# Performance work log

Hardware: AMD Instinct MI355X
Metric: run time of the kernel (lower is better)

The kernel has to match this reference:

```python
import jax, jax.numpy as jnp
import numpy as np

ALPHA = 1.5      # entmax parameter from __init__
N_ITER = 50      # bisection iterations (converges well past fp32 precision)


def entmax_bisect(x, alpha=ALPHA, n_iter=N_ITER):
    """alpha-entmax along the last axis via bisection on the threshold tau.
    p_i = ((alpha-1)*x_i - tau)_+ ** (1/(alpha-1)), with sum_i p_i = 1.
    """
    q = 1.0 / (alpha - 1.0)
    z = x * (alpha - 1.0)
    mx = jnp.max(z, axis=-1, keepdims=True)
    # tau is bracketed by [mx - 1, mx]: sum >= 1 at lo, sum = 0 at hi
    lo, hi = mx - 1.0, mx

    def body(_, carry):
        lo, hi = carry
        tau = 0.5 * (lo + hi)
        f = jnp.sum(jnp.maximum(z - tau, 0.0) ** q, axis=-1, keepdims=True) - 1.0
        lo = jnp.where(f > 0.0, tau, lo)
        hi = jnp.where(f > 0.0, hi, tau)
        return lo, hi

    lo, hi = jax.lax.fori_loop(0, n_iter, body, (lo, hi))
    tau = 0.5 * (lo + hi)
    p = jnp.maximum(z - tau, 0.0) ** q
    return p / jnp.sum(p, axis=-1, keepdims=True)  # exact renormalization


def setup_inputs() -> dict:
    key = jax.random.key(0)
    kq, kk, kv = jax.random.split(key, 3)
    B, T, D = 16, 2048, 256
    return {
        "query": jax.random.normal(kq, (B, T, D), dtype=jnp.float32),
        "value": jax.random.normal(kv, (B, T, D), dtype=jnp.float32),
        "key": jax.random.normal(kk, (B, T, D), dtype=jnp.float32),
    }


def reference(query, value, key):
    # scores: [B, Tq, Tk]
    scores = jnp.einsum("btd,bsd->bts", query, key)
    weights = entmax_bisect(scores)          # sparse attention weights
    return jnp.einsum("bts,bsd->btd", weights, value)
```

## Files before the change

kernel.cpp:

```cpp
#include <hip/hip_runtime.h>

#define TT 2048
#define DD 256
#define RQB 128
#define NT 512
#define KB 128
#define NTILE (TT / KB)
#define NITER 30
#define CAP 28

#define L_CIDX 131072
#define L_CVAL (L_CIDX + RQB * CAP * 2)
#define L_CNT  (L_CVAL + RQB * CAP * 4)
#define L_SLOT (L_CNT + RQB * 4)
#define L_OVF  (L_SLOT + 8 * 16 * CAP * 2)
#define LDS_SZ (L_OVF + 16)

typedef __attribute__((ext_vector_type(4))) float f32x4;
typedef __attribute__((ext_vector_type(8))) short short8;

__device__ inline unsigned short f2bf(float x) {
    unsigned u = __float_as_uint(x);
    return (unsigned short)((u + 0x7fffu + ((u >> 16) & 1u)) >> 16);
}
__device__ inline float bf2f(unsigned short h) {
    return __uint_as_float((unsigned)h << 16);
}

__device__ __forceinline__ void gload16(const void* g, void* l) {
    __builtin_amdgcn_global_load_lds(
        (const __attribute__((address_space(1))) void*)g,
        (__attribute__((address_space(3))) void*)l, 16, 0, 0);
}

__device__ __forceinline__ float dppmax16(float m) {
    int a = __builtin_amdgcn_update_dpp(__float_as_int(m), __float_as_int(m),
                                        0xB1, 0xF, 0xF, false);
    m = fmaxf(m, __int_as_float(a));
    a = __builtin_amdgcn_update_dpp(__float_as_int(m), __float_as_int(m),
                                    0x4E, 0xF, 0xF, false);
    m = fmaxf(m, __int_as_float(a));
    a = __builtin_amdgcn_update_dpp(__float_as_int(m), __float_as_int(m),
                                    0x141, 0xF, 0xF, false);
    m = fmaxf(m, __int_as_float(a));
    a = __builtin_amdgcn_update_dpp(__float_as_int(m), __float_as_int(m),
                                    0x140, 0xF, 0xF, false);
    m = fmaxf(m, __int_as_float(a));
    return m;
}

__global__ __launch_bounds__(256) void split_k_kernel(const float* __restrict__ K,
        unsigned short* __restrict__ Kh, int n4) {
    int i = blockIdx.x * 256 + threadIdx.x;
    const int stride = gridDim.x * 256;
    for (; i < n4; i += stride) {
        float4 v = ((const float4*)K)[i];
        unsigned short h0 = f2bf(0.5f * v.x), h1 = f2bf(0.5f * v.y);
        unsigned short h2 = f2bf(0.5f * v.z), h3 = f2bf(0.5f * v.w);
        uint2 hv;
        hv.x = (unsigned)h0 | ((unsigned)h1 << 16);
        hv.y = (unsigned)h2 | ((unsigned)h3 << 16);
        ((uint2*)Kh)[i] = hv;
    }
}

__launch_bounds__(NT, 2)
__global__ void entmax_screen_kernel(const float* __restrict__ Q,
                                     const unsigned short* __restrict__ Kh,
                                     const float* __restrict__ Kf,
                                     const float* __restrict__ V,
                                     float* __restrict__ Out,
                                     int nwg) {
    extern __shared__ char smem[];
    unsigned short* CIDX = (unsigned short*)(smem + L_CIDX);
    float*          CVAL = (float*)(smem + L_CVAL);
    int*            CNT  = (int*)(smem + L_CNT);
    unsigned short* SLOT = (unsigned short*)(smem + L_SLOT);
    int*            POVF = (int*)(smem + L_OVF);

    const int tid = threadIdx.x;
    const int wid = tid >> 6, lane = tid & 63;
    const int l15 = lane & 15, ag = lane >> 4;
    const int wrow0 = wid * 16;

    const int lb = (blockIdx.x & 7) * (nwg >> 3) + (blockIdx.x >> 3);
    const int b  = lb >> 4;
    const int t0 = (lb & 15) * RQB;

    const char* KhB = (const char*)(Kh + (size_t)b * TT * DD);

    if (tid == 0) *POVF = 0;

    short8 ah[8];
    {
        const float* qr = Q + (size_t)(b * TT + t0 + wrow0 + l15) * DD;
        #pragma unroll
        for (int kk = 0; kk < 8; ++kk) {
            const int d0 = kk * 32 + ag * 8;
            float4 qa = *(const float4*)(qr + d0);
            float4 qb = *(const float4*)(qr + d0 + 4);
            float qf[8] = {qa.x, qa.y, qa.z, qa.w, qb.x, qb.y, qb.z, qb.w};
            #pragma unroll
            for (int i = 0; i < 8; ++i) ah[kk][i] = (short)f2bf(qf[i]);
        }
    }

    auto STAGE = [&](int tile, int buf) {
        #pragma unroll
        for (int j = 0; j < 8; ++j) {
            const int ofs = wid * 8192 + j * 1024 + lane * 16;
            const int cl = ofs >> 9, wb = ofs & 511;
            const size_t gb = ((size_t)((tile << 7) + cl) << 9) +
                              (size_t)(wb ^ ((cl & 7) << 4));
            gload16(KhB + gb, smem + buf * 65536 + wid * 8192 + j * 1024);
        }
    };

    STAGE(0, 0);
    __syncthreads();

    const unsigned long long grpmask = 0xFFFFULL << (ag * 16);
    const unsigned long long lowmask = (lane == 0) ? 0ULL : ((~0ULL) >> (64 - lane));
    float rmax[4];
    int   base[4];
    #pragma unroll
    for (int r = 0; r < 4; ++r) { rmax[r] = -3.402823466e38f; base[r] = 0; }

    for (int t = 0; t < NTILE; ++t) {
        const int cur = t & 1;
        if (t + 1 < NTILE) STAGE(t + 1, cur ^ 1);
        f32x4 acc[8];
        #pragma unroll
        for (int ct = 0; ct < 8; ++ct)
            #pragma unroll
            for (int r = 0; r < 4; ++r) acc[ct][r] = 0.0f;
        #pragma unroll
        for (int kk = 0; kk < 8; ++kk) {
            short8 bh[8];
            #pragma unroll
            for (int ct = 0; ct < 8; ++ct)
                bh[ct] = *(const short8*)(smem + cur * 65536 + (ct * 16 + l15) * 512 +
                                          (((kk * 64) + ag * 16) ^ ((l15 & 7) << 4)));
            #pragma unroll
            for (int ct = 0; ct < 8; ++ct)
                acc[ct] = __builtin_amdgcn_mfma_f32_16x16x32_bf16(ah[kk], bh[ct], acc[ct], 0, 0, 0);
        }
        #pragma unroll
        for (int rg = 0; rg < 4; ++rg) {
            float m = acc[0][rg];
            #pragma unroll
            for (int ct = 1; ct < 8; ++ct) m = fmaxf(m, acc[ct][rg]);
            m = dppmax16(m);
            rmax[rg] = fmaxf(rmax[rg], m);
            const float thr = rmax[rg] - 1.6f;
            if (m > thr) {
                const int row = wrow0 + ag * 4 + rg;
                #pragma unroll
                for (int ct = 0; ct < 8; ++ct) {
                    const bool p = acc[ct][rg] > thr;
                    const unsigned long long ball = __ballot(p) & grpmask;
                    if (ball) {
                        const int rank = (int)__popcll(ball & lowmask);
                        if (p && base[rg] + rank < CAP)
                            CIDX[row * CAP + base[rg] + rank] =
                                (unsigned short)((t << 7) + ct * 16 + l15);
                        base[rg] += (int)__popcll(ball);
                    }
                }
            }
        }
        __syncthreads();
    }

    #pragma unroll
    for (int rg = 0; rg < 4; ++rg) {
        if (l15 == 0) {
            CNT[wrow0 + ag * 4 + rg] = base[rg];
            if (base[rg] > CAP) *POVF = 1;
        }
    }
    __syncthreads();

    int c = 0;
    if (lane < 16) {
        const int cc = CNT[wrow0 + lane];
        c = cc > CAP ? CAP : cc;
    }
    int x = c;
    #pragma unroll
    for (int off = 1; off < 16; off <<= 1) {
        const int v = __shfl_up(x, off);
        if ((lane & 15) >= off) x += v;
    }
    const int pfx = x - c;
    const int total = __shfl(x, 15);
    if (lane < 16)
        for (int i = 0; i < c; ++i)
            SLOT[wid * (16 * CAP) + pfx + i] = (unsigned short)((lane << 8) | i);
    __syncthreads();

    {
        const float* Qb = Q + (size_t)(b * TT + t0 + wrow0) * DD;
        const float* Kb = Kf + (size_t)b * TT * DD;
        for (int bs = 0; bs < total; bs += 8) {
            float4 qv[8], kv[8];
            int rl[8], ii[8];
            #pragma unroll
            for (int u = 0; u < 8; ++u) {
                const int s = bs + u;
                const int e = (s < total) ? (int)SLOT[wid * (16 * CAP) + s] : 0;
                rl[u] = e >> 8; ii[u] = e & 255;
                const int col = (s < total) ? (int)CIDX[(wrow0 + rl[u]) * CAP + ii[u]] : 0;
                qv[u] = *(const float4*)(Qb + (size_t)rl[u] * DD + lane * 4);
                kv[u] = *(const float4*)(Kb + (size_t)col * DD + lane * 4);
            }
            float sm[8];
            #pragma unroll
            for (int u = 0; u < 8; ++u) {
                float d = qv[u].x * kv[u].x;
                d = fmaf(qv[u].y, kv[u].y, d);
                d = fmaf(qv[u].z, kv[u].z, d);
                d = fmaf(qv[u].w, kv[u].w, d);
                sm[u] = d;
            }
            #pragma unroll
            for (int off = 32; off; off >>= 1)
                #pragma unroll
                for (int u = 0; u < 8; ++u) sm[u] += __shfl_xor(sm[u], off);
            #pragma unroll
            for (int u = 0; u < 8; ++u)
                if (lane == u && bs + u < total)
                    CVAL[(wrow0 + rl[u]) * CAP + ii[u]] = 0.5f * sm[u];
        }
    }
    __syncthreads();

    if (*POVF) {
        if (wid == 0) {
            float* fbz = (float*)smem;
            for (int r = 0; r < RQB; ++r) {
                if (CNT[r] <= CAP) continue;
                const float* qr = Q + (size_t)(b * TT + t0 + r) * DD;
                const float* Kb = Kf + (size_t)b * TT * DD;
                for (int cc2 = lane; cc2 < TT; cc2 += 64) {
                    const float* kr = Kb + (size_t)cc2 * DD;
                    float a = 0.0f;
                    for (int d = 0; d < DD; ++d) a = fmaf(qr[d], kr[d], a);
                    fbz[cc2] = 0.5f * a;
                }
                __threadfence_block();
                float m = -3.402823466e38f;
                for (int cc2 = lane; cc2 < TT; cc2 += 64) m = fmaxf(m, fbz[cc2]);
                #pragma unroll
                for (int off = 32; off; off >>= 1) m = fmaxf(m, __shfl_xor(m, off));
                float lo = m - 1.0f, hi = m, tau;
                for (int it = 0; it < NITER; ++it) {
                    tau = 0.5f * (lo + hi);
                    float s = 0.0f;
                    for (int cc2 = lane; cc2 < TT; cc2 += 64) {
                        const float tt2 = fmaxf(fbz[cc2] - tau, 0.0f);
                        s = fmaf(tt2, tt2, s);
                    }
                    #pragma unroll
                    for (int off = 32; off; off >>= 1) s += __shfl_xor(s, off);
                    const bool gt = s > 1.0f;
                    lo = gt ? tau : lo;
                    hi = gt ? hi : tau;
                }
                tau = 0.5f * (lo + hi);
                float ssum = 0.0f;
                for (int cc2 = lane; cc2 < TT; cc2 += 64) {
                    const float tt2 = fmaxf(fbz[cc2] - tau, 0.0f);
                    ssum = fmaf(tt2, tt2, ssum);
                }
                #pragma unroll
                for (int off = 32; off; off >>= 1) ssum += __shfl_xor(ssum, off);
                const float inv = 1.0f / ssum;
                const int d4 = lane * 4;
                float4 o = make_float4(0.f, 0.f, 0.f, 0.f);
                for (int s = 0; s < TT; ++s) {
                    const float tt2 = fmaxf(fbz[s] - tau, 0.0f);
                    const float w = tt2 * tt2 * inv;
                    if (w > 0.0f) {
                        const float4 v = *(const float4*)(V + ((size_t)b * TT + s) * DD + d4);
                        o.x = fmaf(w, v.x, o.x); o.y = fmaf(w, v.y, o.y);
                        o.z = fmaf(w, v.z, o.z); o.w = fmaf(w, v.w, o.w);
                    }
                }
                *(float4*)(Out + ((size_t)(b * TT + t0 + r)) * DD + d4) = o;
                if (lane == 0) CNT[r] = -1;
                __threadfence_block();
            }
        }
        __syncthreads();
    }

    {
        const int myrow = wrow0 + (lane & 15);
        const int nRaw = CNT[myrow];
        const int n = (nRaw < 0) ? 0 : (nRaw > CAP ? CAP : nRaw);
        float cvr[CAP];
        #pragma unroll
        for (int i = 0; i < CAP; ++i)
            cvr[i] = (i < n) ? CVAL[myrow * CAP + i] : -3.0e30f;
        float emax = cvr[0];
        #pragma unroll
        for (int i = 1; i < CAP; ++i) emax = fmaxf(emax, cvr[i]);
        float lo = emax - 1.0f, hi = emax;
        for (int it = 0; it < NITER; ++it) {
            const float tau = 0.5f * (lo + hi);
            float s = 0.0f;
            #pragma unroll
            for (int i = 0; i < CAP; ++i) {
                const float tt2 = fmaxf(cvr[i] - tau, 0.0f);
                s = fmaf(tt2, tt2, s);
            }
            const bool gt = s > 1.0f;
            lo = gt ? tau : lo;
            hi = gt ? hi : tau;
        }
        const float tau = 0.5f * (lo + hi);
        float ssum = 0.0f;
        #pragma unroll
        for (int i = 0; i < CAP; ++i) {
            const float tt2 = fmaxf(cvr[i] - tau, 0.0f);
            ssum = fmaf(tt2, tt2, ssum);
        }
        const float inv = 1.0f / ssum;
        if (lane < 16 && n > 0) {
            for (int i = 0; i < n; ++i) {
                const float tt2 = fmaxf(cvr[i] - tau, 0.0f);
                CVAL[myrow * CAP + i] = tt2 * tt2 * inv;
            }
        }
    }

    const float* Vb = V + (size_t)b * TT * DD;
    for (int j = 0; j < 16; ++j) {
        const int row = wrow0 + j;
        const int n = CNT[row];
        if (n < 0) continue;
        const int d4 = lane * 4;
        float4 o = make_float4(0.f, 0.f, 0.f, 0.f);
        for (int i = 0; i < n; ++i) {
            const float wi = CVAL[row * CAP + i];
            if (wi > 0.0f) {
                const int si = (int)CIDX[row * CAP + i];
                const float4 v = *(const float4*)(Vb + (size_t)si * DD + d4);
                o.x = fmaf(wi, v.x, o.x); o.y = fmaf(wi, v.y, o.y);
                o.z = fmaf(wi, v.z, o.z); o.w = fmaf(wi, v.w, o.w);
            }
        }
        *(float4*)(Out + ((size_t)(b * TT + t0 + row)) * DD + d4) = o;
    }
}

#define DOT4(A, Kv, Qv) \
    A = fmaf((Qv).x, (Kv).x, fmaf((Qv).y, (Kv).y, fmaf((Qv).z, (Kv).z, fmaf((Qv).w, (Kv).w, (A)))))

__launch_bounds__(256, 2)
__global__ void entmax_fallback_kernel(const float* __restrict__ Q,
                                       const float* __restrict__ V,
                                       const float* __restrict__ K,
                                       float* __restrict__ Out) {
    extern __shared__ float zshf[];
    const int tid = threadIdx.x;
    const int b   = blockIdx.x >> 8;
    const int t0  = (blockIdx.x & 255) * 8;
    const float* Qb = Q + ((size_t)b * TT + t0) * DD;
    const float* Kb = K + (size_t)b * TT * DD;
    const float* Vb = V + (size_t)b * TT * DD;
    for (int g = 0; g < 2; ++g) {
        const int c0 = (g << 10) + tid;
        const float* k0 = Kb + (size_t)c0 * DD;
        float4 acc[8];
        #pragma unroll
        for (int r = 0; r < 8; ++r) acc[r] = make_float4(0.f, 0.f, 0.f, 0.f);
        for (int d = 0; d < DD; d += 4) {
            const float4 ka = *(const float4*)(k0 + d);
            const float4 kb = *(const float4*)(k0 + 256 * DD + d);
            const float4 kc = *(const float4*)(k0 + 512 * DD + d);
            const float4 kd = *(const float4*)(k0 + 768 * DD + d);
            #pragma unroll
            for (int r = 0; r < 8; ++r) {
                const float4 qv = *(const float4*)(Qb + r * DD + d);
                DOT4(acc[r].x, ka, qv); DOT4(acc[r].y, kb, qv);
                DOT4(acc[r].z, kc, qv); DOT4(acc[r].w, kd, qv);
            }
        }
        #pragma unroll
        for (int r = 0; r < 8; ++r) {
            zshf[r * TT + c0      ] = 0.5f * acc[r].x;
            zshf[r * TT + c0 + 256] = 0.5f * acc[r].y;
            zshf[r * TT + c0 + 512] = 0.5f * acc[r].z;
            zshf[r * TT + c0 + 768] = 0.5f * acc[r].w;
        }
    }
    __syncthreads();
    {
        const int wid = tid >> 6, lane = tid & 63;
        for (int rr = 0; rr < 2; ++rr) {
            const int r = wid * 2 + rr;
            float* z = zshf + r * TT;
            float zv[32];
            float m = -3.402823466e38f;
            #pragma unroll
            for (int j = 0; j < 32; ++j) { zv[j] = z[lane + (j << 6)]; m = fmaxf(m, zv[j]); }
            #pragma unroll
            for (int off = 32; off; off >>= 1) m = fmaxf(m, __shfl_xor(m, off));
            float lo = m - 1.0f, hi = m;
            for (int it = 0; it < NITER; ++it) {
                const float tau = 0.5f * (lo + hi);
                float s = 0.f;
                #pragma unroll
                for (int j = 0; j < 32; ++j) { float t = fmaxf(zv[j] - tau, 0.f); s = fmaf(t, t, s); }
                #pragma unroll
                for (int off = 32; off; off >>= 1) s += __shfl_xor(s, off);
                const bool gt = (s - 1.0f) > 0.0f;
                lo = gt ? tau : lo; hi = gt ? hi : tau;
            }
            const float tau = 0.5f * (lo + hi);
            float ssum = 0.f;
            #pragma unroll
            for (int j = 0; j < 32; ++j) { float t = fmaxf(zv[j] - tau, 0.f); ssum = fmaf(t, t, ssum); }
            #pragma unroll
            for (int off = 32; off; off >>= 1) ssum += __shfl_xor(ssum, off);
            const float inv = 1.0f / ssum;
            #pragma unroll
            for (int j = 0; j < 32; ++j) {
                float t = fmaxf(zv[j] - tau, 0.f);
                z[lane + (j << 6)] = t * t * inv;
            }
        }
    }
    __syncthreads();
    {
        const int d2 = (tid & 127) * 2;
        const int sg = tid >> 7;
        float2 acc[8];
        #pragma unroll
        for (int r = 0; r < 8; ++r) acc[r] = make_float2(0.f, 0.f);
        for (int sc = 0; sc < TT; sc += 8) {
            const int s0 = sc + sg * 4;
            float4 w4[8];
            #pragma unroll
            for (int r = 0; r < 8; ++r) w4[r] = *(const float4*)&zshf[r * TT + s0];
            #pragma unroll
            for (int js = 0; js < 4; ++js) {
                const float2 v = *(const float2*)(Vb + (size_t)(s0 + js) * DD + d2);
                #pragma unroll
                for (int r = 0; r < 8; ++r) {
                    const float wv = (js == 0) ? w4[r].x : (js == 1) ? w4[r].y
                                   : (js == 2) ? w4[r].z : w4[r].w;
                    acc[r].x = fmaf(wv, v.x, acc[r].x);
                    acc[r].y = fmaf(wv, v.y, acc[r].y);
                }
            }
        }
        __syncthreads();
        float* part = zshf;
        if (sg == 1) {
            #pragma unroll
            for (int r = 0; r < 8; ++r) *(float2*)&part[r * DD + d2] = acc[r];
        }
        __syncthreads();
        if (sg == 0) {
            #pragma unroll
            for (int r = 0; r < 8; ++r) {
                const float2 p = *(const float2*)&part[r * DD + d2];
                float2 o; o.x = acc[r].x + p.x; o.y = acc[r].y + p.y;
                *(float2*)&Out[((size_t)b * TT + t0 + r) * DD + d2] = o;
            }
        }
    }
}

extern "C" void kernel_launch(void* const* d_in, const int* in_sizes, int n_in,
                              void* d_out, int out_size, void* d_ws, size_t ws_size,
                              hipStream_t stream) {
    const float* Q = (const float*)d_in[0];
    const float* V = (const float*)d_in[1];
    const float* K = (const float*)d_in[2];
    float* Out = (float*)d_out;
    const int B = in_sizes[0] / (TT * DD);
    const size_t NE = (size_t)B * TT * DD;
    const size_t need = NE * 2;

    if (ws_size < need) {
        entmax_fallback_kernel<<<dim3(B * (TT / 8)), 256, 8 * TT * sizeof(float), stream>>>(
            Q, V, K, Out);
        return;
    }

    unsigned short* Kh = (unsigned short*)d_ws;
    split_k_kernel<<<2048, 256, 0, stream>>>(K, Kh, (int)(NE / 4));

    const int nwg = B * (TT / RQB);
    (void)hipFuncSetAttribute((const void*)entmax_screen_kernel,
                              hipFuncAttributeMaxDynamicSharedMemorySize, LDS_SZ);
    entmax_screen_kernel<<<dim3(nwg), NT, LDS_SZ, stream>>>(Q, Kh, K, V, Out, nwg);
}
```

Baseline: 135.0 us.

## Triple-buffer smaller K tiles with prefetch depth two and fine-grained waits

```diff
diff --git a/kernel.cpp b/kernel.cpp
--- a/kernel.cpp
+++ b/kernel.cpp
@@ -4,12 +4,12 @@
 #define DD 256
 #define RQB 128
 #define NT 512
-#define KB 128
+#define KB 64
 #define NTILE (TT / KB)
 #define NITER 30
 #define CAP 28
 
-#define L_CIDX 131072
+#define L_CIDX 98304
 #define L_CVAL (L_CIDX + RQB * CAP * 2)
 #define L_CNT  (L_CVAL + RQB * CAP * 4)
 #define L_SLOT (L_CNT + RQB * 4)
@@ -22,9 +22,6 @@
 __device__ inline unsigned short f2bf(float x) {
     unsigned u = __float_as_uint(x);
     return (unsigned short)((u + 0x7fffu + ((u >> 16) & 1u)) >> 16);
-}
-__device__ inline float bf2f(unsigned short h) {
-    return __uint_as_float((unsigned)h << 16);
 }
 
 __device__ __forceinline__ void gload16(const void* g, void* l) {
@@ -105,19 +102,25 @@
         }
     }
 
+    int gofs[4], lofs[4];
+    #pragma unroll
+    for (int j = 0; j < 4; ++j) {
+        const int ofs = wid * 4096 + j * 1024 + lane * 16;
+        const int cl = ofs >> 9, wb = ofs & 511;
+        gofs[j] = cl * 512 + (wb ^ ((cl & 7) << 4));
+        lofs[j] = ofs;
+    }
     auto STAGE = [&](int tile, int buf) {
-        #pragma unroll
-        for (int j = 0; j < 8; ++j) {
-            const int ofs = wid * 8192 + j * 1024 + lane * 16;
-            const int cl = ofs >> 9, wb = ofs & 511;
-            const size_t gb = ((size_t)((tile << 7) + cl) << 9) +
-                              (size_t)(wb ^ ((cl & 7) << 4));
-            gload16(KhB + gb, smem + buf * 65536 + wid * 8192 + j * 1024);
-        }
+        const size_t gt = (size_t)tile << 15;
+        char* lb_ = smem + buf * 32768;
+        #pragma unroll
+        for (int j = 0; j < 4; ++j) gload16(KhB + gt + gofs[j], lb_ + lofs[j]);
     };
 
     STAGE(0, 0);
-    __syncthreads();
+    STAGE(1, 1);
+    asm volatile("s_waitcnt vmcnt(4)" ::: "memory");
+    __builtin_amdgcn_s_barrier();
 
     const unsigned long long grpmask = 0xFFFFULL << (ag * 16);
     const unsigned long long lowmask = (lane == 0) ? 0ULL : ((~0ULL) >> (64 - lane));
@@ -126,50 +129,60 @@
     #pragma unroll
     for (int r = 0; r < 4; ++r) { rmax[r] = -3.402823466e38f; base[r] = 0; }
 
+    int bufc = 0;
     for (int t = 0; t < NTILE; ++t) {
-        const int cur = t & 1;
-        if (t + 1 < NTILE) STAGE(t + 1, cur ^ 1);
-        f32x4 acc[8];
-        #pragma unroll
-        for (int ct = 0; ct < 8; ++ct)
+        if (t + 2 < NTILE) {
+            int sb = bufc + 2; if (sb >= 3) sb -= 3;
+            STAGE(t + 2, sb);
+        }
+        f32x4 acc[4];
+        #pragma unroll
+        for (int ct = 0; ct < 4; ++ct)
             #pragma unroll
             for (int r = 0; r < 4; ++r) acc[ct][r] = 0.0f;
+        __builtin_amdgcn_s_setprio(1);
         #pragma unroll
         for (int kk = 0; kk < 8; ++kk) {
-            short8 bh[8];
-            #pragma unroll
-            for (int ct = 0; ct < 8; ++ct)
-                bh[ct] = *(const short8*)(smem + cur * 65536 + (ct * 16 + l15) * 512 +
+            short8 bh[4];
+            #pragma unroll
+            for (int ct = 0; ct < 4; ++ct)
+                bh[ct] = *(const short8*)(smem + bufc * 32768 + (ct * 16 + l15) * 512 +
                                           (((kk * 64) + ag * 16) ^ ((l15 & 7) << 4)));
             #pragma unroll
-            for (int ct = 0; ct < 8; ++ct)
+            for (int ct = 0; ct < 4; ++ct)
                 acc[ct] = __builtin_amdgcn_mfma_f32_16x16x32_bf16(ah[kk], bh[ct], acc[ct], 0, 0, 0);
         }
+        __builtin_amdgcn_s_setprio(0);
         #pragma unroll
         for (int rg = 0; rg < 4; ++rg) {
-            float m = acc[0][rg];
-            #pragma unroll
-            for (int ct = 1; ct < 8; ++ct) m = fmaxf(m, acc[ct][rg]);
+            float m = fmaxf(fmaxf(acc[0][rg], acc[1][rg]), fmaxf(acc[2][rg], acc[3][rg]));
             m = dppmax16(m);
             rmax[rg] = fmaxf(rmax[rg], m);
             const float thr = rmax[rg] - 1.6f;
             if (m > thr) {
                 const int row = wrow0 + ag * 4 + rg;
                 #pragma unroll
-                for (int ct = 0; ct < 8; ++ct) {
+                for (int ct = 0; ct < 4; ++ct) {
                     const bool p = acc[ct][rg] > thr;
                     const unsigned long long ball = __ballot(p) & grpmask;
                     if (ball) {
                         const int rank = (int)__popcll(ball & lowmask);
                         if (p && base[rg] + rank < CAP)
                             CIDX[row * CAP + base[rg] + rank] =
-                                (unsigned short)((t << 7) + ct * 16 + l15);
+                                (unsigned short)((t << 6) + ct * 16 + l15);
                         base[rg] += (int)__popcll(ball);
                     }
                 }
             }
         }
-        __syncthreads();
+        if (t + 2 < NTILE) {
+            asm volatile("s_waitcnt vmcnt(4)" ::: "memory");
+            __builtin_amdgcn_s_barrier();
+        } else if (t + 2 == NTILE) {
+            asm volatile("s_waitcnt vmcnt(0)" ::: "memory");
+            __builtin_amdgcn_s_barrier();
+        }
+        if (++bufc == 3) bufc = 0;
     }
 
     #pragma unroll
```

After: 145.9 us. +8.1%, slower.

## Switch screening GEMM to 32x32x16 MFMA with 2x2 wave tiling and per-wave candidate merge

Applied to the files above, without the earlier changes.

```diff
diff --git a/kernel.cpp b/kernel.cpp
--- a/kernel.cpp
+++ b/kernel.cpp
@@ -7,24 +7,26 @@
 #define KB 128
 #define NTILE (TT / KB)
 #define NITER 30
-#define CAP 28
-
-#define L_CIDX 131072
-#define L_CVAL (L_CIDX + RQB * CAP * 2)
-#define L_CNT  (L_CVAL + RQB * CAP * 4)
-#define L_SLOT (L_CNT + RQB * 4)
-#define L_OVF  (L_SLOT + 8 * 16 * CAP * 2)
+#define CAPW 20
+#define CAP 40
+#define SLACK 1.6f
+
+#define L_IW   131072
+#define L_CIDX (L_IW + 8 * 32 * CAPW * 2)
+#define L_CW   (L_CIDX + RQB * CAP * 2)
+#define L_OVF  (L_CW + 1024)
 #define LDS_SZ (L_OVF + 16)
-
-typedef __attribute__((ext_vector_type(4))) float f32x4;
+#define L_CVAL 0
+#define L_SLOT 20480
+#define L_CNT  30720
+#define L_FBZ  36864
+
+typedef __attribute__((ext_vector_type(16))) float f32x16;
 typedef __attribute__((ext_vector_type(8))) short short8;
 
 __device__ inline unsigned short f2bf(float x) {
     unsigned u = __float_as_uint(x);
     return (unsigned short)((u + 0x7fffu + ((u >> 16) & 1u)) >> 16);
-}
-__device__ inline float bf2f(unsigned short h) {
-    return __uint_as_float((unsigned)h << 16);
 }
 
 __device__ __forceinline__ void gload16(const void* g, void* l) {
@@ -65,126 +67,156 @@
 }
 
 __launch_bounds__(NT, 2)
-__global__ void entmax_screen_kernel(const float* __restrict__ Q,
-                                     const unsigned short* __restrict__ Kh,
-                                     const float* __restrict__ Kf,
-                                     const float* __restrict__ V,
-                                     float* __restrict__ Out,
-                                     int nwg) {
+__global__ void entmax32_kernel(const float* __restrict__ Q,
+                                const unsigned short* __restrict__ Kh,
+                                const float* __restrict__ Kf,
+                                const float* __restrict__ V,
+                                float* __restrict__ Out,
+                                int nwg) {
     extern __shared__ char smem[];
+    unsigned short* IW   = (unsigned short*)(smem + L_IW);
     unsigned short* CIDX = (unsigned short*)(smem + L_CIDX);
+    int*            CW   = (int*)(smem + L_CW);
+    int*            POVF = (int*)(smem + L_OVF);
     float*          CVAL = (float*)(smem + L_CVAL);
+    unsigned short* SLOT = (unsigned short*)(smem + L_SLOT);
     int*            CNT  = (int*)(smem + L_CNT);
-    unsigned short* SLOT = (unsigned short*)(smem + L_SLOT);
-    int*            POVF = (int*)(smem + L_OVF);
 
     const int tid = threadIdx.x;
     const int wid = tid >> 6, lane = tid & 63;
-    const int l15 = lane & 15, ag = lane >> 4;
-    const int wrow0 = wid * 16;
+    const int l31 = lane & 31, h = lane >> 5;
+    const int rg = wid >> 1, cg = wid & 1;
 
     const int lb = (blockIdx.x & 7) * (nwg >> 3) + (blockIdx.x >> 3);
     const int b  = lb >> 4;
     const int t0 = (lb & 15) * RQB;
 
     const char* KhB = (const char*)(Kh + (size_t)b * TT * DD);
-
     if (tid == 0) *POVF = 0;
 
-    short8 ah[8];
+    short8 ah[16];
     {
-        const float* qr = Q + (size_t)(b * TT + t0 + wrow0 + l15) * DD;
-        #pragma unroll
-        for (int kk = 0; kk < 8; ++kk) {
-            const int d0 = kk * 32 + ag * 8;
-            float4 qa = *(const float4*)(qr + d0);
-            float4 qb = *(const float4*)(qr + d0 + 4);
-            float qf[8] = {qa.x, qa.y, qa.z, qa.w, qb.x, qb.y, qb.z, qb.w};
-            #pragma unroll
-            for (int i = 0; i < 8; ++i) ah[kk][i] = (short)f2bf(qf[i]);
-        }
-    }
-
+        const float* qr = Q + (size_t)(b * TT + t0 + rg * 32 + l31) * DD;
+        #pragma unroll
+        for (int ks = 0; ks < 16; ++ks) {
+            const int d0 = ks * 16 + h * 8;
+            float4 a = *(const float4*)(qr + d0);
+            float4 c = *(const float4*)(qr + d0 + 4);
+            float qf[8] = {a.x, a.y, a.z, a.w, c.x, c.y, c.z, c.w};
+            #pragma unroll
+            for (int i = 0; i < 8; ++i) ah[ks][i] = (short)f2bf(qf[i]);
+        }
+    }
+
+    int gofs[8];
+    #pragma unroll
+    for (int j = 0; j < 8; ++j) {
+        const int ofs = wid * 8192 + j * 1024 + lane * 16;
+        const int cl = ofs >> 9, wb = ofs & 511;
+        gofs[j] = cl * 512 + (wb ^ ((cl & 15) << 4));
+    }
     auto STAGE = [&](int tile, int buf) {
-        #pragma unroll
-        for (int j = 0; j < 8; ++j) {
-            const int ofs = wid * 8192 + j * 1024 + lane * 16;
-            const int cl = ofs >> 9, wb = ofs & 511;
-            const size_t gb = ((size_t)((tile << 7) + cl) << 9) +
-                              (size_t)(wb ^ ((cl & 7) << 4));
-            gload16(KhB + gb, smem + buf * 65536 + wid * 8192 + j * 1024);
-        }
+        const size_t gt = (size_t)tile << 16;
+        char* lb_ = smem + buf * 65536 + wid * 8192;
+        #pragma unroll
+        for (int j = 0; j < 8; ++j) gload16(KhB + gt + gofs[j], lb_ + j * 1024);
     };
 
     STAGE(0, 0);
     __syncthreads();
 
-    const unsigned long long grpmask = 0xFFFFULL << (ag * 16);
-    const unsigned long long lowmask = (lane == 0) ? 0ULL : ((~0ULL) >> (64 - lane));
-    float rmax[4];
-    int   base[4];
+    float rmax[16];
+    int   bs[16];
     #pragma unroll
-    for (int r = 0; r < 4; ++r) { rmax[r] = -3.402823466e38f; base[r] = 0; }
+    for (int r = 0; r < 16; ++r) { rmax[r] = -3.0e30f; bs[r] = 0; }
+
+    const int sx   = (lane & 15) << 4;
+    const int colb = cg * 32768 + l31 * 512;
+    const int koff = h * 16;
 
     for (int t = 0; t < NTILE; ++t) {
         const int cur = t & 1;
         if (t + 1 < NTILE) STAGE(t + 1, cur ^ 1);
-        f32x4 acc[8];
-        #pragma unroll
-        for (int ct = 0; ct < 8; ++ct)
-            #pragma unroll
-            for (int r = 0; r < 4; ++r) acc[ct][r] = 0.0f;
-        #pragma unroll
-        for (int kk = 0; kk < 8; ++kk) {
-            short8 bh[8];
-            #pragma unroll
-            for (int ct = 0; ct < 8; ++ct)
-                bh[ct] = *(const short8*)(smem + cur * 65536 + (ct * 16 + l15) * 512 +
-                                          (((kk * 64) + ag * 16) ^ ((l15 & 7) << 4)));
-            #pragma unroll
-            for (int ct = 0; ct < 8; ++ct)
-                acc[ct] = __builtin_amdgcn_mfma_f32_16x16x32_bf16(ah[kk], bh[ct], acc[ct], 0, 0, 0);
-        }
-        #pragma unroll
-        for (int rg = 0; rg < 4; ++rg) {
-            float m = acc[0][rg];
-            #pragma unroll
-            for (int ct = 1; ct < 8; ++ct) m = fmaxf(m, acc[ct][rg]);
+        const char* tb = smem + cur * 65536 + colb;
+        f32x16 acc0, acc1;
+        #pragma unroll
+        for (int r = 0; r < 16; ++r) { acc0[r] = 0.0f; acc1[r] = 0.0f; }
+        #pragma unroll
+        for (int ks = 0; ks < 16; ++ks) {
+            const int kb = (ks * 32 + koff) ^ sx;
+            const short8 b0 = *(const short8*)(tb + kb);
+            const short8 b1 = *(const short8*)(tb + 16384 + kb);
+            acc0 = __builtin_amdgcn_mfma_f32_32x32x16_bf16(ah[ks], b0, acc0, 0, 0, 0);
+            acc1 = __builtin_amdgcn_mfma_f32_32x32x16_bf16(ah[ks], b1, acc1, 0, 0, 0);
+        }
+        #pragma unroll
+        for (int r = 0; r < 16; ++r) {
+            float m = fmaxf(acc0[r], acc1[r]);
             m = dppmax16(m);
-            rmax[rg] = fmaxf(rmax[rg], m);
-            const float thr = rmax[rg] - 1.6f;
+            m = fmaxf(m, __shfl_xor(m, 16));
+            rmax[r] = fmaxf(rmax[r], m);
+            const float thr = rmax[r] - SLACK;
             if (m > thr) {
-                const int row = wrow0 + ag * 4 + rg;
-                #pragma unroll
-                for (int ct = 0; ct < 8; ++ct) {
-                    const bool p = acc[ct][rg] > thr;
-                    const unsigned long long ball = __ballot(p) & grpmask;
-                    if (ball) {
-                        const int rank = (int)__popcll(ball & lowmask);
-                        if (p && base[rg] + rank < CAP)
-                            CIDX[row * CAP + base[rg] + rank] =
-                                (unsigned short)((t << 7) + ct * 16 + l15);
-                        base[rg] += (int)__popcll(ball);
+                const int lrow = (r & 3) + 8 * (r >> 2) + 4 * h;
+                const int iwb = (wid * 32 + lrow) * CAPW;
+                {
+                    const bool p = acc0[r] > thr;
+                    const unsigned long long ball = __ballot(p);
+                    const unsigned mym = (unsigned)(ball >> (h * 32));
+                    if (mym) {
+                        const int rank = __popc(mym & ((1u << l31) - 1u));
+                        if (p && bs[r] + rank < CAPW)
+                            IW[iwb + bs[r] + rank] =
+                                (unsigned short)(t * KB + cg * 64 + l31);
+                        bs[r] += __popc(mym);
                     }
                 }
+                {
+                    const bool p = acc1[r] > thr;
+                    const unsigned long long ball = __ballot(p);
+                    const unsigned mym = (unsigned)(ball >> (h * 32));
+                    if (mym) {
+                        const int rank = __popc(mym & ((1u << l31) - 1u));
+                        if (p && bs[r] + rank < CAPW)
+                            IW[iwb + bs[r] + rank] =
+                                (unsigned short)(t * KB + cg * 64 + 32 + l31);
+                        bs[r] += __popc(mym);
+                    }
+                }
             }
         }
         __syncthreads();
     }
 
-    #pragma unroll
-    for (int rg = 0; rg < 4; ++rg) {
-        if (l15 == 0) {
-            CNT[wrow0 + ag * 4 + rg] = base[rg];
-            if (base[rg] > CAP) *POVF = 1;
+    if (l31 == 0) {
+        #pragma unroll
+        for (int r = 0; r < 16; ++r) {
+            const int lrow = (r & 3) + 8 * (r >> 2) + 4 * h;
+            CW[wid * 32 + lrow] = bs[r];
         }
     }
     __syncthreads();
+
+    if (lane < 16) {
+        const int row = wid * 16 + lane;
+        const int lr = row & 31;
+        const int w0 = (row >> 5) * 2;
+        int n = 0, ovf = 0;
+        #pragma unroll
+        for (int wv = 0; wv < 2; ++wv) {
+            int cw = CW[(w0 + wv) * 32 + lr];
+            if (cw > CAPW) { ovf = 1; cw = CAPW; }
+            for (int i = 0; i < cw; ++i)
+                CIDX[row * CAP + (n++)] = IW[((w0 + wv) * 32 + lr) * CAPW + i];
+        }
+        CNT[row] = ovf ? (CAP + 1) : n;
+        if (ovf) *POVF = 1;
+    }
 
     int c = 0;
     if (lane < 16) {
-        const int cc = CNT[wrow0 + lane];
-        c = cc > CAP ? CAP : cc;
+        const int cc = CNT[wid * 16 + lane];
+        c = (cc > CAP) ? 0 : cc;
     }
     int x = c;
     #pragma unroll
@@ -197,17 +229,17 @@
     if (lane < 16)
         for (int i = 0; i < c; ++i)
             SLOT[wid * (16 * CAP) + pfx + i] = (unsigned short)((lane << 8) | i);
-    __syncthreads();
 
     {
+        const int wrow0 = wid * 16;
         const float* Qb = Q + (size_t)(b * TT + t0 + wrow0) * DD;
         const float* Kb = Kf + (size_t)b * TT * DD;
-        for (int bs = 0; bs < total; bs += 8) {
+        for (int bsx = 0; bsx < total; bsx += 8) {
             float4 qv[8], kv[8];
             int rl[8], ii[8];
             #pragma unroll
             for (int u = 0; u < 8; ++u) {
-                const int s = bs + u;
+                const int s = bsx + u;
                 const int e = (s < total) ? (int)SLOT[wid * (16 * CAP) + s] : 0;
                 rl[u] = e >> 8; ii[u] = e & 255;
                 const int col = (s < total) ? (int)CIDX[(wrow0 + rl[u]) * CAP + ii[u]] : 0;
@@ -229,7 +261,7 @@
                 for (int u = 0; u < 8; ++u) sm[u] += __shfl_xor(sm[u], off);
             #pragma unroll
             for (int u = 0; u < 8; ++u)
-                if (lane == u && bs + u < total)
+                if (lane == u && bsx + u < total)
                     CVAL[(wrow0 + rl[u]) * CAP + ii[u]] = 0.5f * sm[u];
         }
     }
@@ -237,7 +269,7 @@
 
     if (*POVF) {
         if (wid == 0) {
-            float* fbz = (float*)smem;
+            float* fbz = (float*)(smem + L_FBZ);
             for (int r = 0; r < RQB; ++r) {
                 if (CNT[r] <= CAP) continue;
                 const float* qr = Q + (size_t)(b * TT + t0 + r) * DD;
@@ -296,9 +328,9 @@
     }
 
     {
-        const int myrow = wrow0 + (lane & 15);
+        const int myrow = wid * 16 + (lane & 15);
         const int nRaw = CNT[myrow];
-        const int n = (nRaw < 0) ? 0 : (nRaw > CAP ? CAP : nRaw);
+        const int n = (nRaw < 0 || nRaw > CAP) ? 0 : nRaw;
         float cvr[CAP];
         #pragma unroll
         for (int i = 0; i < CAP; ++i)
@@ -337,9 +369,9 @@
 
     const float* Vb = V + (size_t)b * TT * DD;
     for (int j = 0; j < 16; ++j) {
-        const int row = wrow0 + j;
+        const int row = wid * 16 + j;
         const int n = CNT[row];
-        if (n < 0) continue;
+        if (n < 0 || n > CAP) continue;
         const int d4 = lane * 4;
         float4 o = make_float4(0.f, 0.f, 0.f, 0.f);
         for (int i = 0; i < n; ++i) {
@@ -496,7 +528,7 @@
     split_k_kernel<<<2048, 256, 0, stream>>>(K, Kh, (int)(NE / 4));
 
     const int nwg = B * (TT / RQB);
-    (void)hipFuncSetAttribute((const void*)entmax_screen_kernel,
+    (void)hipFuncSetAttribute((const void*)entmax32_kernel,
                               hipFuncAttributeMaxDynamicSharedMemorySize, LDS_SZ);
-    entmax_screen_kernel<<<dim3(nwg), NT, LDS_SZ, stream>>>(Q, Kh, K, V, Out, nwg);
-}
+    entmax32_kernel<<<dim3(nwg), NT, LDS_SZ, stream>>>(Q, Kh, K, V, Out, nwg);
+}
```

Result: slower. 494.9 us (+266.7%).
